# Optimization experiments

Hardware: AMD Instinct MI355X
Metric: run time of the kernel (lower is better)

## Reference

```python
import jax, jax.numpy as jnp
import numpy as np
from jax import lax

B, S, D, G, V = 32, 8, 128, 32, 64   # batch, slots, hidden_dim, grid_size, vocab_size
K, ED = 128, 32                       # VQ codebook size, code dim


def _conv(x, w, b, pad):
    # standard Conv2d, NCHW / OIHW
    y = lax.conv_general_dilated(x, w, (1, 1), [(pad, pad), (pad, pad)],
                                 dimension_numbers=('NCHW', 'OIHW', 'NCHW'))
    return y + b[None, :, None, None]


def _convT(x, w, b):
    # ConvTranspose2d(k=5, stride=1, padding=2) == conv with spatially flipped
    # kernel, padding k-1-p = 2, channels swapped (IOHW layout of torch weight).
    y = lax.conv_general_dilated(x, jnp.flip(w, (2, 3)), (1, 1), [(2, 2), (2, 2)],
                                 dimension_numbers=('NCHW', 'IOHW', 'NCHW'))
    return y + b[None, :, None, None]


def _build_grid(h, w):
    ys = jnp.linspace(0.0, 1.0, h)
    xs = jnp.linspace(0.0, 1.0, w)
    gy, gx = jnp.meshgrid(ys, xs, indexing='ij')
    g = jnp.stack([gy, gx], axis=-1)                 # [H,W,2]
    return jnp.concatenate([g, 1.0 - g], axis=-1)    # [H,W,4]


def setup_inputs() -> dict:
    key = jax.random.key(0)
    ks = jax.random.split(key, 20)
    sc = 0.05
    n = lambda k, sh: jax.random.normal(k, sh, jnp.float32) * sc
    return {
        'latent': jax.random.normal(ks[0], (B, S, D), jnp.float32),
        'pos_w': n(ks[1], (D, 4)),            # Linear(4, hidden): [out,in]
        'pos_b': jnp.zeros((D,), jnp.float32),
        'ct1_w': n(ks[2], (D, 64, 5, 5)),     # ConvTranspose2d: [in,out,kH,kW]
        'ct1_b': jnp.zeros((64,), jnp.float32),
        'ct2_w': n(ks[3], (64, 32, 5, 5)),
        'ct2_b': jnp.zeros((32,), jnp.float32),
        'codebook': jax.random.uniform(ks[4], (K, ED), jnp.float32, -1.0 / K, 1.0 / K),
        'c1_w': n(ks[5], (64, 32, 3, 3)),     # Conv2d: [out,in,kH,kW]
        'c1_b': jnp.zeros((64,), jnp.float32),
        'c2_w': n(ks[6], (V, 64, 3, 3)),
        'c2_b': jnp.zeros((V,), jnp.float32),
        'a1_w': n(ks[7], (64, 32, 3, 3)),
        'a1_b': jnp.zeros((64,), jnp.float32),
        'a2_w': n(ks[8], (1, 64, 3, 3)),
        'a2_b': jnp.zeros((1,), jnp.float32),
    }


def _forward(latent, pos_w, pos_b, ct1_w, ct1_b, ct2_w, ct2_b, codebook,
             c1_w, c1_b, c2_w, c2_b, a1_w, a1_b, a2_w, a2_b):
    b, s, d = latent.shape
    # spatial broadcast of slot latents -> [B*S, D, H, W]
    z = jnp.broadcast_to(latent.reshape(b * s, d, 1, 1), (b * s, d, G, G))
    # soft position embedding
    grid = _build_grid(G, G)                                  # [H,W,4]
    pos = (grid @ pos_w.T + pos_b).transpose(2, 0, 1)[None]   # [1,D,H,W]
    z = z + pos
    # ConvTranspose decoder
    h = jax.nn.relu(_convT(z, ct1_w, ct1_b))
    feat = jax.nn.relu(_convT(h, ct2_w, ct2_b))               # [B*S,32,H,W]
    # VQ bottleneck on channel-last features
    fp = feat.transpose(0, 2, 3, 1)                           # [B*S,H,W,32]
    flat = fp.reshape(-1, ED)                                 # [N,32]
    dist = (jnp.sum(flat * flat, axis=1, keepdims=True)
            + jnp.sum(codebook * codebook, axis=1)
            - 2.0 * flat @ codebook.T)                        # [N,K]
    idx = jnp.argmin(dist, axis=1)                            # [N]
    q = codebook[idx].reshape(fp.shape)                       # gather lookup
    e_loss = jnp.mean((lax.stop_gradient(q) - fp) ** 2)
    q_loss = jnp.mean((q - lax.stop_gradient(fp)) ** 2)
    vq_loss = q_loss + 0.25 * e_loss
    q_ste = fp + lax.stop_gradient(q - fp)                    # straight-through
    vq_feat = q_ste.transpose(0, 3, 1, 2)                     # [B*S,32,H,W]
    # heads
    colors = _conv(jax.nn.silu(_conv(vq_feat, c1_w, c1_b, 1)), c2_w, c2_b, 1)
    colors = colors.reshape(b, s, V, G, G)
    alphas = _conv(jax.nn.silu(_conv(feat, a1_w, a1_b, 1)), a2_w, a2_b, 1)
    alphas = alphas.reshape(b, s, 1, G, G)
    alphas_n = jax.nn.softmax(alphas, axis=1)
    recon = jnp.sum(alphas_n * colors, axis=1)                # [B,V,H,W]
    return recon, alphas_n, vq_loss


def reference(latent, pos_w, pos_b, ct1_w, ct1_b, ct2_w, ct2_b, codebook,
              c1_w, c1_b, c2_w, c2_b, a1_w, a1_b, a2_w, a2_b):
    return _forward(latent, pos_w, pos_b, ct1_w, ct1_b, ct2_w, ct2_b, codebook,
                    c1_w, c1_b, c2_w, c2_b, a1_w, a1_b, a2_w, a2_b)
```

## Files before the change

### kernel.cpp

```cpp
#include <hip/hip_runtime.h>
#include <math.h>

#define AOFF 2097152
#define LOFF 2359296

typedef __attribute__((ext_vector_type(8))) short short8;
typedef __attribute__((ext_vector_type(4))) float f32x4;

__device__ __forceinline__ int clsf(int v) { return v < 2 ? v : (v > 29 ? v - 27 : 2); }

__device__ __forceinline__ unsigned int f2bfu(float x) {
    unsigned int u = __float_as_uint(x);
    return (u + 0x7FFFu + ((u >> 16) & 1u)) >> 16;
}
__device__ __forceinline__ unsigned int cvt2(float a, float b) {
    return f2bfu(a) | (f2bfu(b) << 16);
}
__device__ __forceinline__ float bf2f(unsigned short u) {
    return __uint_as_float(((unsigned int)u) << 16);
}

__global__ void tapabc_kernel(const float* __restrict__ pw, const float* __restrict__ pb,
                              const float* __restrict__ w1, float* __restrict__ tapabc) {
    __shared__ float A3[384];
    __shared__ float wl[8192];
    int tap = blockIdx.x, t = threadIdx.x;
    if (t < 128) {
        float p0 = pw[t * 4], p1 = pw[t * 4 + 1], p2 = pw[t * 4 + 2], p3 = pw[t * 4 + 3];
        A3[t] = p2 + p3 + pb[t];
        A3[128 + t] = p0 - p2;
        A3[256 + t] = p1 - p3;
    }
    for (int e = t; e < 8192; e += 192) wl[e] = w1[e * 25 + tap];
    __syncthreads();
    int o = t & 63, comp = t >> 6;
    const float* a = A3 + comp * 128;
    float s = 0.f;
    for (int i = 0; i < 128; ++i) s = fmaf(wl[i * 64 + o], a[i], s);
    tapabc[(tap * 64 + o) * 3 + comp] = s;
}

__global__ void pfill_kernel(const float* __restrict__ tapabc, const float* __restrict__ b1,
                             float* __restrict__ P2) {
    __shared__ float uv[75];
    int o = blockIdx.x, t = threadIdx.x;
    if (t < 75) {
        int cls = t / 3, comp = t % 3;
        int cy = cls / 5, cx = cls % 5;
        const int klo[5] = {2, 1, 0, 0, 0}, khi[5] = {4, 4, 4, 3, 2};
        const float inv31 = 1.f / 31.f;
        float s = (comp == 0) ? b1[o] : 0.f;
        for (int ky = klo[cy]; ky <= khi[cy]; ++ky)
            for (int kx = klo[cx]; kx <= khi[cx]; ++kx) {
                int tap = (4 - ky) * 5 + (4 - kx);
                const float* tp = &tapabc[(tap * 64 + o) * 3];
                if (comp == 0) s += tp[0] + tp[1] * (ky - 2) * inv31 + tp[2] * (kx - 2) * inv31;
                else if (comp == 1) s += tp[1] * inv31;
                else s += tp[2] * inv31;
            }
        uv[t] = s;
    }
    __syncthreads();
    int y = t >> 5, x = t & 31;
    int cls = clsf(y) * 5 + clsf(x);
    float val = uv[cls * 3] + uv[cls * 3 + 1] * y + uv[cls * 3 + 2] * x;
    P2[((o >> 1) << 11) + (t << 1) + (o & 1)] = val;
}

__global__ void prep_ws_kernel(const float* __restrict__ w1,
                               const float* __restrict__ a1w, const float* __restrict__ c1w,
                               const float* __restrict__ c2w, const float* __restrict__ ct2w,
                               float* __restrict__ Wsum, short* __restrict__ wtall) {
    int gid = blockIdx.x * 256 + threadIdx.x;
    const int klo[5] = {2, 1, 0, 0, 0}, khi[5] = {4, 4, 4, 3, 2};
    if (gid < 204800) {
        int idx = gid;
        int cls = idx >> 13;
        int i = (idx >> 6) & 127;
        int o = idx & 63;
        int cy = cls / 5, cx = cls % 5;
        float s = 0.f;
        for (int ky = klo[cy]; ky <= khi[cy]; ++ky)
            for (int kx = klo[cx]; kx <= khi[cx]; ++kx)
                s += w1[(i * 64 + o) * 25 + (4 - ky) * 5 + (4 - kx)];
        Wsum[idx] = s;
        return;
    }
    gid -= 204800;
    if (gid < 36864) {
        const float* src = gid < 18432 ? a1w : c1w;
        int idx = gid < 18432 ? gid : gid - 18432;
        int j = idx & 7, fi = idx >> 3;
        int o = fi % 64, g = (fi / 64) & 3, t = fi / 256;
        int i = g * 8 + j;
        wtall[gid] = (short)f2bfu(src[(o * 32 + i) * 9 + (t / 3) * 3 + (t % 3)]);
    } else if (gid < 73728) {
        int idx = gid - 36864;
        int j = idx & 7, fi = idx >> 3;
        int o = fi % 64, g = (fi / 64) & 3, ks = (fi / 256) & 1, t = fi / 512;
        int i = ks * 32 + g * 8 + j;
        wtall[gid] = (short)f2bfu(c2w[(o * 64 + i) * 9 + (t / 3) * 3 + (t % 3)]);
    } else if (gid < 124928) {
        int idx = gid - 73728;
        int j = idx & 7, fi = idx >> 3;
        int o = fi & 31, g = (fi >> 5) & 3, ks = (fi >> 7) & 1, t = fi >> 8;
        int i = ks * 32 + g * 8 + j;
        int ky = t / 5, kx = t % 5;
        wtall[gid] = (short)f2bfu(ct2w[((i * 32 + o) * 5 + (4 - ky)) * 5 + (4 - kx)]);
    }
}

__global__ void m_kernel(const float* __restrict__ latent, const float* __restrict__ Wsum,
                         float* __restrict__ M) {
    int n = blockIdx.x, cls = blockIdx.y, o = threadIdx.x;
    const float* l = &latent[n * 128];
    const float* w = &Wsum[cls * 8192 + o];
    float a0 = 0.f, a1 = 0.f;
    for (int i = 0; i < 128; i += 2) {
        a0 = fmaf(l[i], w[i * 64], a0);
        a1 = fmaf(l[i + 1], w[(i + 1) * 64], a1);
    }
    M[(n * 25 + cls) * 64 + o] = a0 + a1;
}

__global__ __launch_bounds__(256) void conv5_kernel(
        const float* __restrict__ M, const float* __restrict__ P2,
        const short* __restrict__ wt, const float* __restrict__ b2,
        unsigned short* __restrict__ featb) {
    __shared__ __align__(16) short tile[12 * 36 * 40];
    __shared__ float Ml[1600];
    const int n = blockIdx.x, y0 = blockIdx.y * 8;
    const int tid = threadIdx.x, w = tid >> 6, l = tid & 63;
    const int lx = l & 15, lg = l >> 4;

    for (int e = tid; e < 1600; e += 256) Ml[e] = M[n * 1600 + e];
    __syncthreads();

    f32x4 acc[2][2][2];
    #pragma unroll
    for (int m = 0; m < 2; ++m)
        #pragma unroll
        for (int q = 0; q < 2; ++q)
            #pragma unroll
            for (int c = 0; c < 2; ++c) acc[m][q][c] = (f32x4){0.f, 0.f, 0.f, 0.f};

    #pragma unroll 1
    for (int ks = 0; ks < 2; ++ks) {
        if (ks) __syncthreads();
        for (int e = tid; e < 6912; e += 256) {
            int cx = e % 36;
            int q = e / 36;
            int ipl = q & 15;
            int r = q >> 4;
            int gy = y0 - 2 + r, gx = cx - 2;
            unsigned int pack = 0u;
            if (gy >= 0 && gy < 32 && gx >= 0 && gx < 32) {
                int cls = clsf(gy) * 5 + clsf(gx);
                int pp = gy * 32 + gx;
                float2 pv = ((const float2*)P2)[((ks * 16 + ipl) << 10) + pp];
                float2 ml = ((const float2*)Ml)[cls * 32 + ks * 16 + ipl];
                pack = cvt2(fmaxf(ml.x + pv.x, 0.f), fmaxf(ml.y + pv.y, 0.f));
            }
            *(unsigned int*)((char*)tile + (r * 36 + cx) * 80 + ipl * 4) = pack;
        }
        __syncthreads();
        for (int kx = 0; kx < 5; ++kx) {
            short8 af[5][2];
            #pragma unroll
            for (int ky = 0; ky < 5; ++ky)
                #pragma unroll
                for (int m = 0; m < 2; ++m)
                    af[ky][m] = *(const short8*)(wt + (ky * 5 + kx) * 2048 +
                                                 ((ks * 4 + lg) * 32 + m * 16 + lx) * 8);
            #pragma unroll
            for (int colf = 0; colf < 2; ++colf) {
                const int cbase = ((2 * w) * 36 + kx + colf * 16 + lx) * 80 + lg * 16;
                short8 bc[6];
                #pragma unroll
                for (int ir = 0; ir < 6; ++ir)
                    bc[ir] = *(const short8*)((char*)tile + cbase + ir * (36 * 80));
                #pragma unroll
                for (int ky = 0; ky < 5; ++ky)
                    #pragma unroll
                    for (int q = 0; q < 2; ++q)
                        #pragma unroll
                        for (int m = 0; m < 2; ++m)
                            acc[m][q][colf] = __builtin_amdgcn_mfma_f32_16x16x32_bf16(
                                af[ky][m], bc[q + ky], acc[m][q][colf], 0, 0, 0);
            }
        }
    }

    #pragma unroll
    for (int m = 0; m < 2; ++m)
        #pragma unroll
        for (int q = 0; q < 2; ++q)
            #pragma unroll
            for (int colf = 0; colf < 2; ++colf) {
                int yl = 2 * w + q, x = colf * 16 + lx;
                unsigned long long pk = 0ull;
                #pragma unroll
                for (int r = 0; r < 4; ++r) {
                    int och = m * 16 + lg * 4 + r;
                    float v = fmaxf(acc[m][q][colf][r] + b2[och], 0.f);
                    pk |= (unsigned long long)f2bfu(v) << (16 * r);
                }
                *(unsigned long long*)(featb + (n * 1024 + (y0 + yl) * 32 + x) * 32
                                       + m * 16 + lg * 4) = pk;
            }
}

template<int ACT>
__global__ __launch_bounds__(256, 6) void conv3_kernel(
        const unsigned short* __restrict__ in_, const short* __restrict__ wt,
        const float* __restrict__ bias, unsigned short* __restrict__ out_) {
    __shared__ __align__(16) short smem[6 * 34 * 40];
    const int n = blockIdx.x, y0 = blockIdx.y * 4;
    const int tid = threadIdx.x, w = tid >> 6, l = tid & 63;
    const int lx = l & 15, lg = l >> 4;

    for (int e = tid; e < 816; e += 256) {
        int px = e >> 2, qc = e & 3;
        int r = px / 34, cx = px - r * 34;
        int gy = y0 - 1 + r, gx = cx - 1;
        short8 v8 = (short8){0, 0, 0, 0, 0, 0, 0, 0};
        if (gy >= 0 && gy < 32 && gx >= 0 && gx < 32)
            v8 = *(const short8*)(in_ + (n * 1024 + gy * 32 + gx) * 32 + qc * 8);
        *(short8*)((char*)smem + px * 80 + qc * 16) = v8;
    }
    __syncthreads();

    f32x4 acc[4][2];
    #pragma unroll
    for (int m = 0; m < 4; ++m)
        #pragma unroll
        for (int c = 0; c < 2; ++c) acc[m][c] = (f32x4){0.f, 0.f, 0.f, 0.f};

    #pragma unroll
    for (int kx = 0; kx < 3; ++kx) {
        short8 bc[2][3];
        #pragma unroll
        for (int colf = 0; colf < 2; ++colf) {
            const int cbase = (w * 34 + kx + colf * 16 + lx) * 80 + lg * 16;
            #pragma unroll
            for (int ir = 0; ir < 3; ++ir)
                bc[colf][ir] = *(const short8*)((char*)smem + cbase + ir * (34 * 80));
        }
        #pragma unroll
        for (int m = 0; m < 4; ++m) {
            short8 af[3];
            #pragma unroll
            for (int ky = 0; ky < 3; ++ky)
                af[ky] = *(const short8*)(wt + (ky * 3 + kx) * 2048 +
                                          (lg * 64 + m * 16 + lx) * 8);
            #pragma unroll
            for (int ky = 0; ky < 3; ++ky)
                #pragma unroll
                for (int colf = 0; colf < 2; ++colf)
                    acc[m][colf] = __builtin_amdgcn_mfma_f32_16x16x32_bf16(
                        af[ky], bc[colf][ky], acc[m][colf], 0, 0, 0);
        }
    }

    #pragma unroll
    for (int m = 0; m < 4; ++m)
        #pragma unroll
        for (int colf = 0; colf < 2; ++colf) {
            int x = colf * 16 + lx;
            unsigned long long pk = 0ull;
            #pragma unroll
            for (int r = 0; r < 4; ++r) {
                int och = m * 16 + lg * 4 + r;
                float v = acc[m][colf][r] + bias[och];
                if (ACT == 1) v = v / (1.f + expf(-v));
                pk |= (unsigned long long)f2bfu(v) << (16 * r);
            }
            *(unsigned long long*)(out_ + (n * 1024 + (y0 + w) * 32 + x) * 64
                                   + m * 16 + lg * 4) = pk;
        }
}

__global__ __launch_bounds__(256, 6) void conv3a2_kernel(
        const unsigned short* __restrict__ in_, const short* __restrict__ wt,
        const float* __restrict__ bias, const float* __restrict__ a2w,
        float* __restrict__ s9) {
    __shared__ __align__(16) short smem[8192];
    __shared__ float wl9[576];
    const int n = blockIdx.x, y0 = blockIdx.y * 4;
    const int tid = threadIdx.x, w = tid >> 6, l = tid & 63;
    const int lx = l & 15, lg = l >> 4;

    for (int e = tid; e < 576; e += 256) wl9[e] = a2w[e];
    for (int e = tid; e < 816; e += 256) {
        int px = e >> 2, qc = e & 3;
        int r = px / 34, cx = px - r * 34;
        int gy = y0 - 1 + r, gx = cx - 1;
        short8 v8 = (short8){0, 0, 0, 0, 0, 0, 0, 0};
        if (gy >= 0 && gy < 32 && gx >= 0 && gx < 32)
            v8 = *(const short8*)(in_ + (n * 1024 + gy * 32 + gx) * 32 + qc * 8);
        *(short8*)((char*)smem + px * 80 + qc * 16) = v8;
    }
    __syncthreads();

    f32x4 acc[4][2];
    #pragma unroll
    for (int m = 0; m < 4; ++m)
        #pragma unroll
        for (int c = 0; c < 2; ++c) acc[m][c] = (f32x4){0.f, 0.f, 0.f, 0.f};

    #pragma unroll
    for (int kx = 0; kx < 3; ++kx) {
        short8 bc[2][3];
        #pragma unroll
        for (int colf = 0; colf < 2; ++colf) {
            const int cbase = (w * 34 + kx + colf * 16 + lx) * 80 + lg * 16;
            #pragma unroll
            for (int ir = 0; ir < 3; ++ir)
                bc[colf][ir] = *(const short8*)((char*)smem + cbase + ir * (34 * 80));
        }
        #pragma unroll
        for (int m = 0; m < 4; ++m) {
            short8 af[3];
            #pragma unroll
            for (int ky = 0; ky < 3; ++ky)
                af[ky] = *(const short8*)(wt + (ky * 3 + kx) * 2048 +
                                          (lg * 64 + m * 16 + lx) * 8);
            #pragma unroll
            for (int ky = 0; ky < 3; ++ky)
                #pragma unroll
                for (int colf = 0; colf < 2; ++colf)
                    acc[m][colf] = __builtin_amdgcn_mfma_f32_16x16x32_bf16(
                        af[ky], bc[colf][ky], acc[m][colf], 0, 0, 0);
        }
    }

    short8 af9[2];
    #pragma unroll
    for (int ks = 0; ks < 2; ++ks)
        #pragma unroll
        for (int j = 0; j < 8; ++j) {
            int ch = ks * 32 + lg * 8 + j;
            float v = (lx < 9) ? wl9[ch * 9 + lx] : 0.f;
            af9[ks][j] = (short)f2bfu(v);
        }

    __syncthreads();
    char* base = (char*)smem + w * 4096;
    #pragma unroll
    for (int m = 0; m < 4; ++m)
        #pragma unroll
        for (int colf = 0; colf < 2; ++colf) {
            int px = colf * 16 + lx;
            unsigned long long pk = 0ull;
            #pragma unroll
            for (int r = 0; r < 4; ++r) {
                int och = m * 16 + lg * 4 + r;
                float v = acc[m][colf][r] + bias[och];
                v = v / (1.f + expf(-v));
                pk |= (unsigned long long)f2bfu(v) << (16 * r);
            }
            int slot = 2 * m + (lg >> 1);
            int off = px * 128 + (((slot ^ (px & 7)) << 4)) + (lg & 1) * 8;
            *(unsigned long long*)(base + off) = pk;
        }
    __syncthreads();

    #pragma unroll
    for (int colf = 0; colf < 2; ++colf) {
        int px = colf * 16 + lx;
        f32x4 sp = (f32x4){0.f, 0.f, 0.f, 0.f};
        #pragma unroll
        for (int ks = 0; ks < 2; ++ks) {
            int slot = ks * 4 + lg;
            short8 bf = *(const short8*)(base + px * 128 + ((slot ^ (px & 7)) << 4));
            sp = __builtin_amdgcn_mfma_f32_16x16x32_bf16(af9[ks], bf, sp, 0, 0, 0);
        }
        int p = (n << 10) + (y0 + w) * 32 + px;
        #pragma unroll
        for (int r = 0; r < 4; ++r) {
            int t9 = lg * 4 + r;
            if (t9 < 9) s9[(t9 << 18) + p] = sp[r];
        }
    }
}

__global__ __launch_bounds__(256) void c2_kernel(
        const unsigned short* __restrict__ in_, const short* __restrict__ wt,
        const float* __restrict__ bias, unsigned short* __restrict__ out_) {
    __shared__ __align__(16) short smem[10 * 34 * 40];
    const int n = blockIdx.x, y0 = blockIdx.y * 8;
    const int tid = threadIdx.x, w = tid >> 6, l = tid & 63;
    const int lx = l & 15, lg = l >> 4;

    short8 r0[6], r1[6];
    int pxv[6], qcv[6];
    #pragma unroll
    for (int it = 0; it < 6; ++it) {
        int e = tid + it * 256;
        int px = e >> 2, qc = e & 3;
        pxv[it] = px; qcv[it] = qc;
        short8 v0 = (short8){0, 0, 0, 0, 0, 0, 0, 0};
        short8 v1 = v0;
        if (e < 1360) {
            int r = px / 34, cx = px - r * 34;
            int gy = y0 - 1 + r, gx = cx - 1;
            if (gy >= 0 && gy < 32 && gx >= 0 && gx < 32) {
                const unsigned short* p = in_ + (n * 1024 + gy * 32 + gx) * 64 + qc * 8;
                v0 = *(const short8*)p;
                v1 = *(const short8*)(p + 32);
            }
        }
        r0[it] = v0; r1[it] = v1;
    }
    #pragma unroll
    for (int it = 0; it < 6; ++it)
        if (tid + it * 256 < 1360)
            *(short8*)((char*)smem + pxv[it] * 80 + qcv[it] * 16) = r0[it];
    __syncthreads();

    f32x4 acc[4][2][2];
    #pragma unroll
    for (int m = 0; m < 4; ++m)
        #pragma unroll
        for (int q = 0; q < 2; ++q)
            #pragma unroll
            for (int c = 0; c < 2; ++c) acc[m][q][c] = (f32x4){0.f, 0.f, 0.f, 0.f};

    #pragma unroll
    for (int kx = 0; kx < 3; ++kx) {
        short8 af[3][4];
        #pragma unroll
        for (int ky = 0; ky < 3; ++ky)
            #pragma unroll
            for (int m = 0; m < 4; ++m)
                af[ky][m] = *(const short8*)(wt + (ky * 3 + kx) * 4096 +
                                             (lg * 64 + m * 16 + lx) * 8);
        #pragma unroll
        for (int colf = 0; colf < 2; ++colf) {
            const int cbase = ((2 * w) * 34 + kx + colf * 16 + lx) * 80 + lg * 16;
            short8 bc[4];
            #pragma unroll
            for (int ir = 0; ir < 4; ++ir)
                bc[ir] = *(const short8*)((char*)smem + cbase + ir * (34 * 80));
            #pragma unroll
            for (int ky = 0; ky < 3; ++ky)
                #pragma unroll
                for (int q = 0; q < 2; ++q)
                    #pragma unroll
                    for (int m = 0; m < 4; ++m)
                        acc[m][q][colf] = __builtin_amdgcn_mfma_f32_16x16x32_bf16(
                            af[ky][m], bc[q + ky], acc[m][q][colf], 0, 0, 0);
        }
    }
    __syncthreads();
    #pragma unroll
    for (int it = 0; it < 6; ++it)
        if (tid + it * 256 < 1360)
            *(short8*)((char*)smem + pxv[it] * 80 + qcv[it] * 16) = r1[it];
    __syncthreads();
    #pragma unroll
    for (int kx = 0; kx < 3; ++kx) {
        short8 af[3][4];
        #pragma unroll
        for (int ky = 0; ky < 3; ++ky)
            #pragma unroll
            for (int m = 0; m < 4; ++m)
                af[ky][m] = *(const short8*)(wt + (ky * 3 + kx) * 4096 +
                                             ((4 + lg) * 64 + m * 16 + lx) * 8);
        #pragma unroll
        for (int colf = 0; colf < 2; ++colf) {
            const int cbase = ((2 * w) * 34 + kx + colf * 16 + lx) * 80 + lg * 16;
            short8 bc[4];
            #pragma unroll
            for (int ir = 0; ir < 4; ++ir)
                bc[ir] = *(const short8*)((char*)smem + cbase + ir * (34 * 80));
            #pragma unroll
            for (int ky = 0; ky < 3; ++ky)
                #pragma unroll
                for (int q = 0; q < 2; ++q)
                    #pragma unroll
                    for (int m = 0; m < 4; ++m)
                        acc[m][q][colf] = __builtin_amdgcn_mfma_f32_16x16x32_bf16(
                            af[ky][m], bc[q + ky], acc[m][q][colf], 0, 0, 0);
        }
    }

    #pragma unroll
    for (int m = 0; m < 4; ++m)
        #pragma unroll
        for (int q = 0; q < 2; ++q)
            #pragma unroll
            for (int colf = 0; colf < 2; ++colf) {
                int yl = 2 * w + q, x = colf * 16 + lx;
                unsigned long long pk = 0ull;
                #pragma unroll
                for (int r = 0; r < 4; ++r) {
                    int och = m * 16 + lg * 4 + r;
                    float v = acc[m][q][colf][r] + bias[och];
                    pk |= (unsigned long long)f2bfu(v) << (16 * r);
                }
                *(unsigned long long*)(out_ + (n * 1024 + (y0 + yl) * 32 + x) * 64
                                       + m * 16 + lg * 4) = pk;
            }
}

__global__ void a2soft_kernel(const float* __restrict__ s9, const float* __restrict__ b2,
                              float* __restrict__ outp) {
    int idx = blockIdx.x * 256 + threadIdx.x;
    if (idx >= 32 * 1024) return;
    int bb = idx >> 10, yx = idx & 1023;
    int y = yx >> 5, x = yx & 31;
    float v[8];
    float bias = b2[0];
    #pragma unroll
    for (int s = 0; s < 8; ++s) {
        int n = bb * 8 + s;
        float a = bias;
        #pragma unroll
        for (int ky = 0; ky < 3; ++ky) {
            int yy = y + ky - 1;
            if (yy < 0 || yy > 31) continue;
            #pragma unroll
            for (int kx = 0; kx < 3; ++kx) {
                int xx = x + kx - 1;
                if (xx < 0 || xx > 31) continue;
                a += s9[((ky * 3 + kx) << 18) + (n << 10) + yy * 32 + xx];
            }
        }
        v[s] = a;
    }
    float m = -3.4e38f;
    #pragma unroll
    for (int s = 0; s < 8; ++s) m = fmaxf(m, v[s]);
    float sum = 0.f;
    #pragma unroll
    for (int s = 0; s < 8; ++s) { v[s] = expf(v[s] - m); sum += v[s]; }
    float inv = 1.f / sum;
    #pragma unroll
    for (int s = 0; s < 8; ++s) outp[AOFF + ((bb * 8 + s) << 10) + yx] = v[s] * inv;
}

__global__ __launch_bounds__(256) void vq_mfma_kernel(
        const unsigned short* __restrict__ featb, const float* __restrict__ codebook,
        unsigned short* __restrict__ qfeat, float* __restrict__ partial) {
    __shared__ float cbf[4096];
    __shared__ __align__(16) short cbh[4096];
    __shared__ float cn[128];
    __shared__ float red[4];
    const int tid = threadIdx.x;
    const int w = tid >> 6, l = tid & 63;
    const int lx = l & 15, lg = l >> 4;

    for (int e = tid; e < 4096; e += 256) {
        float v = codebook[e];
        cbf[e] = v;
        int code = e >> 5, d = e & 31;
        int off = (code * 32 + d) * 2;
        off ^= (code & 7) << 4;
        *(short*)((char*)cbh + off) = (short)f2bfu(v);
    }
    __syncthreads();
    if (tid < 128) {
        float s = 0.f;
        #pragma unroll
        for (int c = 0; c < 32; ++c) { float v = cbf[tid * 32 + c]; s = fmaf(v, v, s); }
        cn[tid] = s;
    }
    short8 af[8];
    #pragma unroll
    for (int m = 0; m < 8; ++m) {
        int code = m * 16 + lx;
        int off = (code * 32 + lg * 8) * 2;
        off ^= (code & 7) << 4;
        af[m] = *(const short8*)((char*)cbh + off);
    }
    __syncthreads();
    float cnh[8][4];
    #pragma unroll
    for (int m = 0; m < 8; ++m)
        #pragma unroll
        for (int r = 0; r < 4; ++r)
            cnh[m][r] = 0.5f * cn[m * 16 + lg * 4 + r];

    const int n = blockIdx.x >> 2;
    const int yxw = (blockIdx.x & 3) * 256 + w * 64;
    float lloss = 0.f;

    #pragma unroll 1
    for (int pxg = 0; pxg < 4; ++pxg) {
        int yx = yxw + pxg * 16 + lx;
        short8 bbs = *(const short8*)(featb + (n * 1024 + yx) * 32 + lg * 8);
        f32x4 S[8];
        #pragma unroll
        for (int m = 0; m < 8; ++m)
            S[m] = __builtin_amdgcn_mfma_f32_16x16x32_bf16(
                af[m], bbs, (f32x4){0.f, 0.f, 0.f, 0.f}, 0, 0, 0);
        float bestv = -3.4e38f; int besti = 0;
        #pragma unroll
        for (int m = 0; m < 8; ++m)
            #pragma unroll
            for (int r = 0; r < 4; ++r) {
                float v = S[m][r] - cnh[m][r];
                int code = m * 16 + lg * 4 + r;
                if (v > bestv) { bestv = v; besti = code; }
            }
        #pragma unroll
        for (int d = 16; d < 64; d <<= 1) {
            float ov = __shfl_xor(bestv, d);
            int oi = __shfl_xor(besti, d);
            if (ov > bestv || (ov == bestv && oi < besti)) { bestv = ov; besti = oi; }
        }
        int offq = (besti * 32 + lg * 8) * 2;
        offq ^= (besti & 7) << 4;
        short8 qh = *(const short8*)((char*)cbh + offq);
        *(short8*)(qfeat + (n * 1024 + yx) * 32 + lg * 8) = qh;
        const float* qf = &cbf[besti * 32 + lg * 8];
        #pragma unroll
        for (int j = 0; j < 8; ++j) {
            float fv = bf2f((unsigned short)bbs[j]);
            float dd = qf[j] - fv;
            lloss = fmaf(dd, dd, lloss);
        }
    }
    for (int off = 32; off > 0; off >>= 1) lloss += __shfl_down(lloss, off);
    if (l == 0) red[w] = lloss;
    __syncthreads();
    if (tid == 0) partial[blockIdx.x] = (red[0] + red[1]) + (red[2] + red[3]);
}

__global__ __launch_bounds__(256) void recon_kernel(
        const unsigned short* __restrict__ colors, float* __restrict__ outp) {
    const int b = blockIdx.x, y8 = blockIdx.y;
    const int tid = threadIdx.x;
    const int yxl = tid & 127, vh = tid >> 7;
    const int yx = y8 * 128 + yxl;
    float acc[32];
    #pragma unroll
    for (int v = 0; v < 32; ++v) acc[v] = 0.f;
    #pragma unroll 1
    for (int s = 0; s < 8; ++s) {
        float a = outp[AOFF + ((b * 8 + s) << 10) + yx];
        const unsigned short* cp = colors + ((b * 8 + s) * 1024 + yx) * 64 + vh * 32;
        #pragma unroll
        for (int k = 0; k < 4; ++k) {
            short8 v8 = *(const short8*)(cp + k * 8);
            #pragma unroll
            for (int j = 0; j < 8; ++j)
                acc[k * 8 + j] = fmaf(a, bf2f((unsigned short)v8[j]), acc[k * 8 + j]);
        }
    }
    #pragma unroll
    for (int v = 0; v < 32; ++v)
        outp[(b * 64 + vh * 32 + v) * 1024 + yx] = acc[v];
}

__global__ void loss_kernel(const float* __restrict__ partial, float* __restrict__ outp) {
    __shared__ float red[4];
    int t = threadIdx.x;
    float s = 0.f;
    for (int i = t; i < 1024; i += 256) s += partial[i];
    for (int o = 32; o > 0; o >>= 1) s += __shfl_down(s, o);
    if ((t & 63) == 0) red[t >> 6] = s;
    __syncthreads();
    if (t == 0) outp[LOFF] = 1.25f * ((red[0] + red[1]) + (red[2] + red[3])) / 8388608.0f;
}

extern "C" void kernel_launch(void* const* d_in, const int* in_sizes, int n_in,
                              void* d_out, int out_size, void* d_ws, size_t ws_size,
                              hipStream_t stream) {
    const float* latent  = (const float*)d_in[0];
    const float* pos_w   = (const float*)d_in[1];
    const float* pos_b   = (const float*)d_in[2];
    const float* ct1_w   = (const float*)d_in[3];
    const float* ct1_b   = (const float*)d_in[4];
    const float* ct2_w   = (const float*)d_in[5];
    const float* ct2_b   = (const float*)d_in[6];
    const float* codebook= (const float*)d_in[7];
    const float* c1_w    = (const float*)d_in[8];
    const float* c1_b    = (const float*)d_in[9];
    const float* c2_w    = (const float*)d_in[10];
    const float* c2_b    = (const float*)d_in[11];
    const float* a1_w    = (const float*)d_in[12];
    const float* a1_b    = (const float*)d_in[13];
    const float* a2_w    = (const float*)d_in[14];
    const float* a2_b    = (const float*)d_in[15];
    float* out = (float*)d_out;

    float* ws     = (float*)d_ws;
    unsigned short* featb = (unsigned short*)ws;
    float* s9     = ws + 8388608;
    float* tapabc = s9 + 2359296;
    float* P      = tapabc + 4800;
    float* M      = P + 65536;
    float* partial= M + 409600;
    float* Wsum   = partial + 1024;
    short* wtall  = (short*)(Wsum + 204800);
    short* wtA    = wtall;
    short* wtC1   = wtall + 18432;
    short* wtC2   = wtall + 36864;
    short* wtT2   = wtall + 73728;
    unsigned short* tmpb    = (unsigned short*)(wtall + 124928);
    unsigned short* qfeatb  = tmpb + 16777216;
    unsigned short* colorsb = qfeatb + 8388608;

    tapabc_kernel<<<25, 192, 0, stream>>>(pos_w, pos_b, ct1_w, tapabc);
    pfill_kernel<<<64, 1024, 0, stream>>>(tapabc, ct1_b, P);
    prep_ws_kernel<<<1288, 256, 0, stream>>>(ct1_w, a1_w, c1_w, c2_w, ct2_w, Wsum, wtall);
    m_kernel<<<dim3(256, 25), 64, 0, stream>>>(latent, Wsum, M);

    conv5_kernel<<<dim3(256, 4), 256, 0, stream>>>(M, P, wtT2, ct2_b, featb);
    conv3a2_kernel<<<dim3(256, 8), 256, 0, stream>>>(featb, wtA, a1_b, a2_w, s9);
    a2soft_kernel<<<128, 256, 0, stream>>>(s9, a2_b, out);
    vq_mfma_kernel<<<1024, 256, 0, stream>>>(featb, codebook, qfeatb, partial);
    conv3_kernel<1><<<dim3(256, 8), 256, 0, stream>>>(qfeatb, wtC1, c1_b, tmpb);
    c2_kernel<<<dim3(256, 4), 256, 0, stream>>>(tmpb, wtC2, c2_b, colorsb);
    recon_kernel<<<dim3(32, 8), 256, 0, stream>>>(colorsb, out);
    loss_kernel<<<1, 256, 0, stream>>>(partial, out);
}
```

Before: 209.2 us.

## Fuse VQ nearest-code search into conv5 epilogue

```diff
diff --git a/kernel.cpp b/kernel.cpp
--- a/kernel.cpp
+++ b/kernel.cpp
@@ -126,14 +126,31 @@
 __global__ __launch_bounds__(256) void conv5_kernel(
         const float* __restrict__ M, const float* __restrict__ P2,
         const short* __restrict__ wt, const float* __restrict__ b2,
-        unsigned short* __restrict__ featb) {
+        const float* __restrict__ codebook,
+        unsigned short* __restrict__ featb, unsigned short* __restrict__ qfeat,
+        float* __restrict__ partial) {
     __shared__ __align__(16) short tile[12 * 36 * 40];
     __shared__ float Ml[1600];
+    __shared__ __align__(16) short cbh[4096];
+    __shared__ float cn[128];
+    __shared__ float red[4];
     const int n = blockIdx.x, y0 = blockIdx.y * 8;
     const int tid = threadIdx.x, w = tid >> 6, l = tid & 63;
     const int lx = l & 15, lg = l >> 4;
 
     for (int e = tid; e < 1600; e += 256) Ml[e] = M[n * 1600 + e];
+    for (int e = tid; e < 4096; e += 256) {
+        int code = e >> 5, d = e & 31;
+        int off = (code * 32 + d) * 2;
+        off ^= (code & 7) << 4;
+        *(short*)((char*)cbh + off) = (short)f2bfu(codebook[e]);
+    }
+    if (tid < 128) {
+        float s = 0.f;
+        #pragma unroll
+        for (int c = 0; c < 32; ++c) { float v = codebook[tid * 32 + c]; s = fmaf(v, v, s); }
+        cn[tid] = s;
+    }
     __syncthreads();
 
     f32x4 acc[2][2][2];
@@ -191,6 +208,8 @@
         }
     }
 
+    __syncthreads();
+    char* base = (char*)tile + w * 5120;
     #pragma unroll
     for (int m = 0; m < 2; ++m)
         #pragma unroll
@@ -205,9 +224,68 @@
                     float v = fmaxf(acc[m][q][colf][r] + b2[och], 0.f);
                     pk |= (unsigned long long)f2bfu(v) << (16 * r);
                 }
-                *(unsigned long long*)(featb + (n * 1024 + (y0 + yl) * 32 + x) * 32
+                *(unsigned long long*)(featb + (n * 1024 + yl * 32 + x + y0 * 32) * 32
                                        + m * 16 + lg * 4) = pk;
-            }
+                int px = q * 32 + colf * 16 + lx;
+                int slot = m * 2 + (lg >> 1);
+                *(unsigned long long*)(base + px * 80 + slot * 16 + (lg & 1) * 8) = pk;
+            }
+
+    short8 af9[8];
+    #pragma unroll
+    for (int m = 0; m < 8; ++m) {
+        int off = ((m * 16 + lx) * 32 + lg * 8) * 2;
+        off ^= (lx & 7) << 4;
+        af9[m] = *(const short8*)((char*)cbh + off);
+    }
+    float cnh[8][4];
+    #pragma unroll
+    for (int m = 0; m < 8; ++m)
+        #pragma unroll
+        for (int r = 0; r < 4; ++r)
+            cnh[m][r] = 0.5f * cn[m * 16 + lg * 4 + r];
+    __syncthreads();
+
+    float lloss = 0.f;
+    #pragma unroll 1
+    for (int g = 0; g < 4; ++g) {
+        int px = g * 16 + lx;
+        short8 bbs = *(const short8*)(base + px * 80 + lg * 16);
+        f32x4 S[8];
+        #pragma unroll
+        for (int m = 0; m < 8; ++m)
+            S[m] = __builtin_amdgcn_mfma_f32_16x16x32_bf16(
+                af9[m], bbs, (f32x4){0.f, 0.f, 0.f, 0.f}, 0, 0, 0);
+        float bestv = -3.4e38f; int besti = 0;
+        #pragma unroll
+        for (int m = 0; m < 8; ++m)
+            #pragma unroll
+            for (int r = 0; r < 4; ++r) {
+                float v = S[m][r] - cnh[m][r];
+                int code = m * 16 + lg * 4 + r;
+                if (v > bestv) { bestv = v; besti = code; }
+            }
+        #pragma unroll
+        for (int d = 16; d < 64; d <<= 1) {
+            float ov = __shfl_xor(bestv, d);
+            int oi = __shfl_xor(besti, d);
+            if (ov > bestv || (ov == bestv && oi < besti)) { bestv = ov; besti = oi; }
+        }
+        int offq = (besti * 32 + lg * 8) * 2;
+        offq ^= (besti & 7) << 4;
+        short8 qh = *(const short8*)((char*)cbh + offq);
+        int yx = (y0 + 2 * w + (px >> 5)) * 32 + (px & 31);
+        *(short8*)(qfeat + (n * 1024 + yx) * 32 + lg * 8) = qh;
+        #pragma unroll
+        for (int j = 0; j < 8; ++j) {
+            float dd = bf2f((unsigned short)qh[j]) - bf2f((unsigned short)bbs[j]);
+            lloss = fmaf(dd, dd, lloss);
+        }
+    }
+    for (int off = 32; off > 0; off >>= 1) lloss += __shfl_down(lloss, off);
+    if (l == 0) red[w] = lloss;
+    __syncthreads();
+    if (tid == 0) partial[blockIdx.y * 256 + n] = (red[0] + red[1]) + (red[2] + red[3]);
 }
 
 template<int ACT>
@@ -538,94 +616,6 @@
     float inv = 1.f / sum;
     #pragma unroll
     for (int s = 0; s < 8; ++s) outp[AOFF + ((bb * 8 + s) << 10) + yx] = v[s] * inv;
-}
-
-__global__ __launch_bounds__(256) void vq_mfma_kernel(
-        const unsigned short* __restrict__ featb, const float* __restrict__ codebook,
-        unsigned short* __restrict__ qfeat, float* __restrict__ partial) {
-    __shared__ float cbf[4096];
-    __shared__ __align__(16) short cbh[4096];
-    __shared__ float cn[128];
-    __shared__ float red[4];
-    const int tid = threadIdx.x;
-    const int w = tid >> 6, l = tid & 63;
-    const int lx = l & 15, lg = l >> 4;
-
-    for (int e = tid; e < 4096; e += 256) {
-        float v = codebook[e];
-        cbf[e] = v;
-        int code = e >> 5, d = e & 31;
-        int off = (code * 32 + d) * 2;
-        off ^= (code & 7) << 4;
-        *(short*)((char*)cbh + off) = (short)f2bfu(v);
-    }
-    __syncthreads();
-    if (tid < 128) {
-        float s = 0.f;
-        #pragma unroll
-        for (int c = 0; c < 32; ++c) { float v = cbf[tid * 32 + c]; s = fmaf(v, v, s); }
-        cn[tid] = s;
-    }
-    short8 af[8];
-    #pragma unroll
-    for (int m = 0; m < 8; ++m) {
-        int code = m * 16 + lx;
-        int off = (code * 32 + lg * 8) * 2;
-        off ^= (code & 7) << 4;
-        af[m] = *(const short8*)((char*)cbh + off);
-    }
-    __syncthreads();
-    float cnh[8][4];
-    #pragma unroll
-    for (int m = 0; m < 8; ++m)
-        #pragma unroll
-        for (int r = 0; r < 4; ++r)
-            cnh[m][r] = 0.5f * cn[m * 16 + lg * 4 + r];
-
-    const int n = blockIdx.x >> 2;
-    const int yxw = (blockIdx.x & 3) * 256 + w * 64;
-    float lloss = 0.f;
-
-    #pragma unroll 1
-    for (int pxg = 0; pxg < 4; ++pxg) {
-        int yx = yxw + pxg * 16 + lx;
-        short8 bbs = *(const short8*)(featb + (n * 1024 + yx) * 32 + lg * 8);
-        f32x4 S[8];
-        #pragma unroll
-        for (int m = 0; m < 8; ++m)
-            S[m] = __builtin_amdgcn_mfma_f32_16x16x32_bf16(
-                af[m], bbs, (f32x4){0.f, 0.f, 0.f, 0.f}, 0, 0, 0);
-        float bestv = -3.4e38f; int besti = 0;
-        #pragma unroll
-        for (int m = 0; m < 8; ++m)
-            #pragma unroll
-            for (int r = 0; r < 4; ++r) {
-                float v = S[m][r] - cnh[m][r];
-                int code = m * 16 + lg * 4 + r;
-                if (v > bestv) { bestv = v; besti = code; }
-            }
-        #pragma unroll
-        for (int d = 16; d < 64; d <<= 1) {
-            float ov = __shfl_xor(bestv, d);
-            int oi = __shfl_xor(besti, d);
-            if (ov > bestv || (ov == bestv && oi < besti)) { bestv = ov; besti = oi; }
-        }
-        int offq = (besti * 32 + lg * 8) * 2;
-        offq ^= (besti & 7) << 4;
-        short8 qh = *(const short8*)((char*)cbh + offq);
-        *(short8*)(qfeat + (n * 1024 + yx) * 32 + lg * 8) = qh;
-        const float* qf = &cbf[besti * 32 + lg * 8];
-        #pragma unroll
-        for (int j = 0; j < 8; ++j) {
-            float fv = bf2f((unsigned short)bbs[j]);
-            float dd = qf[j] - fv;
-            lloss = fmaf(dd, dd, lloss);
-        }
-    }
-    for (int off = 32; off > 0; off >>= 1) lloss += __shfl_down(lloss, off);
-    if (l == 0) red[w] = lloss;
-    __syncthreads();
-    if (tid == 0) partial[blockIdx.x] = (red[0] + red[1]) + (red[2] + red[3]);
 }
 
 __global__ __launch_bounds__(256) void recon_kernel(
@@ -708,10 +698,10 @@
     prep_ws_kernel<<<1288, 256, 0, stream>>>(ct1_w, a1_w, c1_w, c2_w, ct2_w, Wsum, wtall);
     m_kernel<<<dim3(256, 25), 64, 0, stream>>>(latent, Wsum, M);
 
-    conv5_kernel<<<dim3(256, 4), 256, 0, stream>>>(M, P, wtT2, ct2_b, featb);
+    conv5_kernel<<<dim3(256, 4), 256, 0, stream>>>(M, P, wtT2, ct2_b, codebook,
+                                                   featb, qfeatb, partial);
     conv3a2_kernel<<<dim3(256, 8), 256, 0, stream>>>(featb, wtA, a1_b, a2_w, s9);
     a2soft_kernel<<<128, 256, 0, stream>>>(s9, a2_b, out);
-    vq_mfma_kernel<<<1024, 256, 0, stream>>>(featb, codebook, qfeatb, partial);
     conv3_kernel<1><<<dim3(256, 8), 256, 0, stream>>>(qfeatb, wtC1, c1_b, tmpb);
     c2_kernel<<<dim3(256, 4), 256, 0, stream>>>(tmpb, wtC2, c2_b, colorsb);
     recon_kernel<<<dim3(32, 8), 256, 0, stream>>>(colorsb, out);
```

Result: slower. 224.8 us (+7.4%).
